# Performance work log

Measured on AMD Instinct MI355X. Metric: run time of the kernel, lower is better.

## Reference

```python
import jax, jax.numpy as jnp
import numpy as np

H = 64  # rnn_hidden_size


def _rnn_seq(x, W_ih, W_hh, b_ih, b_hh):
    """One tanh RNN layer over [B,T,D] -> full output sequence [B,T,H]."""
    pre = jnp.einsum('btd,hd->bth', x, W_ih) + b_ih  # input projection hoisted out of the scan
    h0 = jnp.zeros((x.shape[0], W_hh.shape[0]), x.dtype)
    def step(h, p_t):
        h = jnp.tanh(p_t + h @ W_hh.T + b_hh)
        return h, h
    _, ys = jax.lax.scan(step, h0, jnp.swapaxes(pre, 0, 1))  # scan over time
    return jnp.swapaxes(ys, 0, 1)


def _rnn_last(x, W_ih, W_hh, b_ih, b_hh):
    """One tanh RNN layer, returning only the last hidden state [B,H]."""
    pre = jnp.einsum('btd,hd->bth', x, W_ih) + b_ih
    h0 = jnp.zeros((x.shape[0], W_hh.shape[0]), x.dtype)
    def step(h, p_t):
        return jnp.tanh(p_t + h @ W_hh.T + b_hh), None
    h, _ = jax.lax.scan(step, h0, jnp.swapaxes(pre, 0, 1))
    return h


def setup_inputs() -> dict:
    key = jax.random.key(0)
    ks = jax.random.split(key, 32)
    B, T, D = 128, 4096, 3
    kr = 1.0 / np.sqrt(H)          # PyTorch RNN init bound
    u = lambda kk, shape, b: jax.random.uniform(kk, shape, jnp.float32, -b, b)
    inp = {
        'x': jax.random.normal(ks[0], (B, T, D), jnp.float32),
        'y': jax.random.normal(ks[1], (B, T, D), jnp.float32),
        'z': jax.random.normal(ks[2], (5,), jnp.float32),
        # rnn_empty, layer 0 (in=3) and layer 1 (in=64)
        'e_Wih0': u(ks[3], (H, D), kr), 'e_Whh0': u(ks[4], (H, H), kr),
        'e_bih0': u(ks[5], (H,), kr),  'e_bhh0': u(ks[6], (H,), kr),
        'e_Wih1': u(ks[7], (H, H), kr), 'e_Whh1': u(ks[8], (H, H), kr),
        'e_bih1': u(ks[9], (H,), kr),  'e_bhh1': u(ks[10], (H,), kr),
        # rnn_occupied
        'o_Wih0': u(ks[11], (H, D), kr), 'o_Whh0': u(ks[12], (H, H), kr),
        'o_bih0': u(ks[13], (H,), kr),  'o_bhh0': u(ks[14], (H,), kr),
        'o_Wih1': u(ks[15], (H, H), kr), 'o_Whh1': u(ks[16], (H, H), kr),
        'o_bih1': u(ks[17], (H,), kr),  'o_bhh1': u(ks[18], (H,), kr),
        # heads: fce/fco (64->2), fc1 (9->64), fc2 (64->5)
        'fce_w': u(ks[19], (2, H), kr), 'fce_b': u(ks[20], (2,), kr),
        'fco_w': u(ks[21], (2, H), kr), 'fco_b': u(ks[22], (2,), kr),
        'fc1_w': u(ks[23], (64, 9), 1.0 / np.sqrt(9)), 'fc1_b': u(ks[24], (64,), 1.0 / np.sqrt(9)),
        'fc2_w': u(ks[25], (5, 64), kr), 'fc2_b': u(ks[26], (5,), kr),
    }
    return inp


def reference(x, y, z,
              e_Wih0, e_Whh0, e_bih0, e_bhh0, e_Wih1, e_Whh1, e_bih1, e_bhh1,
              o_Wih0, o_Whh0, o_bih0, o_bhh0, o_Wih1, o_Whh1, o_bih1, o_bhh1,
              fce_w, fce_b, fco_w, fco_b, fc1_w, fc1_b, fc2_w, fc2_b):
    # two 2-layer tanh RNNs; last-timestep output of layer 2 == final hidden of layer 2
    hx = _rnn_last(_rnn_seq(x, e_Wih0, e_Whh0, e_bih0, e_bhh0),
                   e_Wih1, e_Whh1, e_bih1, e_bhh1)            # [B,H]
    hy = _rnn_last(_rnn_seq(y, o_Wih0, o_Whh0, o_bih0, o_bhh0),
                   o_Wih1, o_Whh1, o_bih1, o_bhh1)            # [B,H]
    e = hx @ fce_w.T + fce_b                                  # [B,2]
    o = hy @ fco_w.T + fco_b                                  # [B,2]
    zz = jnp.concatenate([e[0], o[0], z])                     # [9]
    h = jax.nn.relu(zz @ fc1_w.T + fc1_b)                     # [64]
    return h @ fc2_w.T + fc2_b                                # [5]
```

## Files before the change

kernel.cpp:

```cpp
#include <hip/hip_runtime.h>

#define T 4096
#define EP 8
#define RING 32
#define NEP (T / EP + 2)

__device__ __forceinline__ float fast_tanh(float x) {
    float e = __expf(2.0f * x);
    float r = __builtin_amdgcn_rcpf(e + 1.0f);
    return fmaf(-2.0f, r, 1.0f);
}

__device__ __forceinline__ float lane_bcast(float v, int j) {
    return __uint_as_float(__builtin_amdgcn_readlane(__float_as_uint(v), j));
}

#define ANCHOR16(a, b) asm volatile("" : \
    "+v"((a)[(b)+0]),  "+v"((a)[(b)+1]),  "+v"((a)[(b)+2]),  "+v"((a)[(b)+3]),  \
    "+v"((a)[(b)+4]),  "+v"((a)[(b)+5]),  "+v"((a)[(b)+6]),  "+v"((a)[(b)+7]),  \
    "+v"((a)[(b)+8]),  "+v"((a)[(b)+9]),  "+v"((a)[(b)+10]), "+v"((a)[(b)+11]), \
    "+v"((a)[(b)+12]), "+v"((a)[(b)+13]), "+v"((a)[(b)+14]), "+v"((a)[(b)+15]))
#define ANCHOR64(a) do { ANCHOR16(a, 0); ANCHOR16(a, 16); \
                         ANCHOR16(a, 32); ANCHOR16(a, 48); } while (0)

__global__ void prep_kernel(const float* __restrict__ x, const float* __restrict__ y,
                            const float* __restrict__ eW, const float* __restrict__ ebi,
                            const float* __restrict__ ebh,
                            const float* __restrict__ oW, const float* __restrict__ obi,
                            const float* __restrict__ obh,
                            float* __restrict__ pre)
{
    int idx = blockIdx.x * blockDim.x + threadIdx.x;
    int i = idx & 63;
    int t = (idx >> 6) & (T - 1);
    int s = idx >> 18;
    const float* in = s ? y : x;
    const float* W  = s ? oW : eW;
    const float* bi = s ? obi : ebi;
    const float* bh = s ? obh : ebh;
    float v = bi[i] + bh[i]
            + W[i*3+0]*in[t*3+0] + W[i*3+1]*in[t*3+1] + W[i*3+2]*in[t*3+2];
    pre[idx] = v;
}

__global__ __launch_bounds__(256, 1) void seq_kernel(
    const float* __restrict__ pre,
    const float* __restrict__ eWhh0, const float* __restrict__ eWih1,
    const float* __restrict__ eWhh1, const float* __restrict__ ebih1,
    const float* __restrict__ ebhh1,
    const float* __restrict__ oWhh0, const float* __restrict__ oWih1,
    const float* __restrict__ oWhh1, const float* __restrict__ obih1,
    const float* __restrict__ obhh1,
    float* __restrict__ hlast)
{
    const int s    = blockIdx.x;
    const int wv   = threadIdx.x >> 6;
    const int lane = threadIdx.x & 63;

    __shared__ __align__(16) float h0ring[RING][64];
    __shared__ __align__(16) float qring[RING][64];

    const float* p = pre + s * T * 64;

    if (wv == 0) {
        const float* Whh0 = s ? oWhh0 : eWhh0;
        float w0[64];
#pragma unroll
        for (int j = 0; j < 64; ++j) w0[j] = Whh0[lane * 64 + j];

        float hp = 0.f;
        float pc[EP], pn[EP];
#pragma unroll
        for (int i = 0; i < EP; ++i) pc[i] = p[i * 64 + lane];

        for (int k = 0; k < NEP; ++k) {
            ANCHOR64(w0);
            const int base = k * EP;
#pragma unroll
            for (int i = 0; i < EP; ++i) {
                int t = base + EP + i;
                pn[i] = (t < T) ? p[t * 64 + lane] : 0.f;
            }
            if (base < T) {
#pragma unroll
                for (int i = 0; i < EP; ++i) {
                    float aa[4] = { pc[i], 0.f, 0.f, 0.f };
#pragma unroll
                    for (int jb = 0; jb < 64; jb += 8) {
                        float hj[8];
#pragma unroll
                        for (int u = 0; u < 8; ++u) hj[u] = lane_bcast(hp, jb + u);
#pragma unroll
                        for (int u = 0; u < 8; ++u)
                            aa[u & 3] = fmaf(w0[jb + u], hj[u], aa[u & 3]);
                    }
                    hp = fast_tanh((aa[0] + aa[1]) + (aa[2] + aa[3]));
                    h0ring[(base + i) & (RING - 1)][lane] = hp;
                }
            }
#pragma unroll
            for (int i = 0; i < EP; ++i) pc[i] = pn[i];
            __syncthreads();
        }
    } else if (wv <= 2) {
        const float* Wih1 = s ? oWih1 : eWih1;
        const float  b1   = s ? (obih1[lane] + obhh1[lane])
                              : (ebih1[lane] + ebhh1[lane]);
        float wi[64];
#pragma unroll
        for (int j = 0; j < 64; ++j) wi[j] = Wih1[lane * 64 + j];

        const int i0 = (wv - 1) * (EP / 2);

        for (int k = 0; k < NEP; ++k) {
            ANCHOR64(wi);
            const int base = k * EP - EP;
            if (base >= 0 && base < T) {
#pragma unroll
                for (int i = 0; i < EP / 2; ++i) {
                    const int t = base + i0 + i;
                    const float4* hv = (const float4*)h0ring[t & (RING - 1)];
                    float q[4] = { b1, 0.f, 0.f, 0.f };
#pragma unroll
                    for (int j4 = 0; j4 < 16; ++j4) {
                        float4 u = hv[j4];
                        q[0] = fmaf(wi[4*j4+0], u.x, q[0]);
                        q[1] = fmaf(wi[4*j4+1], u.y, q[1]);
                        q[2] = fmaf(wi[4*j4+2], u.z, q[2]);
                        q[3] = fmaf(wi[4*j4+3], u.w, q[3]);
                    }
                    qring[t & (RING - 1)][lane] = (q[0] + q[1]) + (q[2] + q[3]);
                }
            }
            __syncthreads();
        }
    } else {
        const float* Whh1 = s ? oWhh1 : eWhh1;
        float w1[64];
#pragma unroll
        for (int j = 0; j < 64; ++j) w1[j] = Whh1[lane * 64 + j];

        float hp = 0.f;
        for (int k = 0; k < NEP; ++k) {
            ANCHOR64(w1);
            const int base = k * EP - 2 * EP;
            if (base >= 0) {
                float qb[EP];
#pragma unroll
                for (int i = 0; i < EP; ++i)
                    qb[i] = qring[(base + i) & (RING - 1)][lane];
#pragma unroll
                for (int i = 0; i < EP; ++i) {
                    float cc[4] = { qb[i], 0.f, 0.f, 0.f };
#pragma unroll
                    for (int jb = 0; jb < 64; jb += 8) {
                        float hj[8];
#pragma unroll
                        for (int u = 0; u < 8; ++u) hj[u] = lane_bcast(hp, jb + u);
#pragma unroll
                        for (int u = 0; u < 8; ++u)
                            cc[u & 3] = fmaf(w1[jb + u], hj[u], cc[u & 3]);
                    }
                    hp = fast_tanh((cc[0] + cc[1]) + (cc[2] + cc[3]));
                }
            }
            __syncthreads();
        }
        hlast[s * 64 + lane] = hp;
    }
}

__global__ void head_kernel(const float* __restrict__ hlast,
                            const float* __restrict__ z,
                            const float* __restrict__ fce_w, const float* __restrict__ fce_b,
                            const float* __restrict__ fco_w, const float* __restrict__ fco_b,
                            const float* __restrict__ fc1_w, const float* __restrict__ fc1_b,
                            const float* __restrict__ fc2_w, const float* __restrict__ fc2_b,
                            float* __restrict__ out)
{
    const int lane = threadIdx.x;
    __shared__ float zz[9];
    __shared__ float hh[64];

    if (lane < 2) {
        float sacc = fce_b[lane];
        for (int j = 0; j < 64; ++j) sacc += fce_w[lane * 64 + j] * hlast[j];
        zz[lane] = sacc;
    } else if (lane < 4) {
        int r = lane - 2;
        float sacc = fco_b[r];
        for (int j = 0; j < 64; ++j) sacc += fco_w[r * 64 + j] * hlast[64 + j];
        zz[lane] = sacc;
    } else if (lane < 9) {
        zz[lane] = z[lane - 4];
    }
    __syncthreads();

    float sacc = fc1_b[lane];
#pragma unroll
    for (int j = 0; j < 9; ++j) sacc += fc1_w[lane * 9 + j] * zz[j];
    hh[lane] = fmaxf(sacc, 0.f);
    __syncthreads();

    if (lane < 5) {
        float o = fc2_b[lane];
        for (int i = 0; i < 64; ++i) o += fc2_w[lane * 64 + i] * hh[i];
        out[lane] = o;
    }
}

extern "C" void kernel_launch(void* const* d_in, const int* in_sizes, int n_in,
                              void* d_out, int out_size, void* d_ws, size_t ws_size,
                              hipStream_t stream)
{
    const float* x      = (const float*)d_in[0];
    const float* y      = (const float*)d_in[1];
    const float* z      = (const float*)d_in[2];
    const float* e_Wih0 = (const float*)d_in[3];
    const float* e_Whh0 = (const float*)d_in[4];
    const float* e_bih0 = (const float*)d_in[5];
    const float* e_bhh0 = (const float*)d_in[6];
    const float* e_Wih1 = (const float*)d_in[7];
    const float* e_Whh1 = (const float*)d_in[8];
    const float* e_bih1 = (const float*)d_in[9];
    const float* e_bhh1 = (const float*)d_in[10];
    const float* o_Wih0 = (const float*)d_in[11];
    const float* o_Whh0 = (const float*)d_in[12];
    const float* o_bih0 = (const float*)d_in[13];
    const float* o_bhh0 = (const float*)d_in[14];
    const float* o_Wih1 = (const float*)d_in[15];
    const float* o_Whh1 = (const float*)d_in[16];
    const float* o_bih1 = (const float*)d_in[17];
    const float* o_bhh1 = (const float*)d_in[18];
    const float* fce_w  = (const float*)d_in[19];
    const float* fce_b  = (const float*)d_in[20];
    const float* fco_w  = (const float*)d_in[21];
    const float* fco_b  = (const float*)d_in[22];
    const float* fc1_w  = (const float*)d_in[23];
    const float* fc1_b  = (const float*)d_in[24];
    const float* fc2_w  = (const float*)d_in[25];
    const float* fc2_b  = (const float*)d_in[26];

    float* pre   = (float*)d_ws;
    float* hlast = pre + 2 * T * 64;
    float* out   = (float*)d_out;

    prep_kernel<<<(2 * T * 64) / 256, 256, 0, stream>>>(
        x, y, e_Wih0, e_bih0, e_bhh0, o_Wih0, o_bih0, o_bhh0, pre);

    seq_kernel<<<2, 256, 0, stream>>>(
        pre,
        e_Whh0, e_Wih1, e_Whh1, e_bih1, e_bhh1,
        o_Whh0, o_Wih1, o_Whh1, o_bih1, o_bhh1,
        hlast);

    head_kernel<<<1, 64, 0, stream>>>(
        hlast, z, fce_w, fce_b, fco_w, fco_b, fc1_w, fc1_b, fc2_w, fc2_b, out);
}
```

Measured before the change: 1.104 ms.

## Replace readlane broadcasts with DPP row-rotate and bpermute in recurrent matvec

The per-step recurrent matvec previously broadcast each of the 64 hidden values with v_readlane into scalar registers, which serializes through SGPRs. It now rotates the hidden vector within 16-lane rows using DPP row_ror fused into the FMAs, and fetches the other three 16-lane quarters with ds_bpermute. The weights are pre-permuted per lane so each rotation matches the right column. The direction of the DPP rotation is detected at runtime to pick the permutation. This adds LDS-crossbar latency from the bpermutes on the serial critical path, plus the risk that the rotation semantics are wrong.

```diff
diff --git a/kernel.cpp b/kernel.cpp
--- a/kernel.cpp
+++ b/kernel.cpp
@@ -9,10 +9,6 @@
     float e = __expf(2.0f * x);
     float r = __builtin_amdgcn_rcpf(e + 1.0f);
     return fmaf(-2.0f, r, 1.0f);
-}
-
-__device__ __forceinline__ float lane_bcast(float v, int j) {
-    return __uint_as_float(__builtin_amdgcn_readlane(__float_as_uint(v), j));
 }
 
 #define ANCHOR16(a, b) asm volatile("" : \
@@ -22,6 +18,47 @@
     "+v"((a)[(b)+12]), "+v"((a)[(b)+13]), "+v"((a)[(b)+14]), "+v"((a)[(b)+15]))
 #define ANCHOR64(a) do { ANCHOR16(a, 0); ANCHOR16(a, 16); \
                          ANCHOR16(a, 32); ANCHOR16(a, 48); } while (0)
+
+#define ROTF(acc, v, w, R) \
+    (acc) = fmaf(__int_as_float(__builtin_amdgcn_update_dpp( \
+        0, __float_as_int(v), 0x120 + (R), 0xF, 0xF, false)), (w), (acc))
+
+#define KBLOCK(v, wd, B) do { \
+    a0 = fmaf((v), (wd)[(B) + 0], a0); \
+    ROTF(a1, (v), (wd)[(B) + 1],  1);  ROTF(a2, (v), (wd)[(B) + 2],  2); \
+    ROTF(a3, (v), (wd)[(B) + 3],  3);  ROTF(a0, (v), (wd)[(B) + 4],  4); \
+    ROTF(a1, (v), (wd)[(B) + 5],  5);  ROTF(a2, (v), (wd)[(B) + 6],  6); \
+    ROTF(a3, (v), (wd)[(B) + 7],  7);  ROTF(a0, (v), (wd)[(B) + 8],  8); \
+    ROTF(a1, (v), (wd)[(B) + 9],  9);  ROTF(a2, (v), (wd)[(B) +10], 10); \
+    ROTF(a3, (v), (wd)[(B) +11], 11);  ROTF(a0, (v), (wd)[(B) +12], 12); \
+    ROTF(a1, (v), (wd)[(B) +13], 13);  ROTF(a2, (v), (wd)[(B) +14], 14); \
+    ROTF(a3, (v), (wd)[(B) +15], 15); \
+} while (0)
+
+__device__ __forceinline__ float rnn_step_dpp(const float (&wd)[64], float init, float hp,
+                                              int a16, int a32, int a48) {
+    const int hb = __float_as_int(hp);
+    const int b1i = __builtin_amdgcn_ds_bpermute(a16, hb);
+    const int b2i = __builtin_amdgcn_ds_bpermute(a32, hb);
+    const int b3i = __builtin_amdgcn_ds_bpermute(a48, hb);
+    float a0 = init, a1 = 0.f, a2 = 0.f, a3 = 0.f;
+    KBLOCK(hp, wd, 0);
+    const float v1 = __int_as_float(b1i); KBLOCK(v1, wd, 16);
+    const float v2 = __int_as_float(b2i); KBLOCK(v2, wd, 32);
+    const float v3 = __int_as_float(b3i); KBLOCK(v3, wd, 48);
+    return fast_tanh((a0 + a1) + (a2 + a3));
+}
+
+__device__ __forceinline__ void load_wdpp(const float* __restrict__ W, int lane,
+                                          bool dirplus, float (&wd)[64]) {
+#pragma unroll
+    for (int m = 0; m < 64; ++m) {
+        const int k = m >> 4, r = m & 15;
+        const int lowoff = dirplus ? r : ((16 - r) & 15);
+        const int j = ((lane & 48) | ((lane + lowoff) & 15)) ^ (k << 4);
+        wd[m] = W[lane * 64 + j];
+    }
+}
 
 __global__ void prep_kernel(const float* __restrict__ x, const float* __restrict__ y,
                             const float* __restrict__ eW, const float* __restrict__ ebi,
@@ -62,11 +99,16 @@
 
     const float* p = pre + s * T * 64;
 
+    const int got = __builtin_amdgcn_update_dpp(0, lane, 0x121, 0xF, 0xF, false);
+    const bool dirplus = ((got & 15) == ((lane + 1) & 15));
+    const int a16 = (lane ^ 16) << 2;
+    const int a32 = (lane ^ 32) << 2;
+    const int a48 = (lane ^ 48) << 2;
+
     if (wv == 0) {
         const float* Whh0 = s ? oWhh0 : eWhh0;
-        float w0[64];
-#pragma unroll
-        for (int j = 0; j < 64; ++j) w0[j] = Whh0[lane * 64 + j];
+        float wd[64];
+        load_wdpp(Whh0, lane, dirplus, wd);
 
         float hp = 0.f;
         float pc[EP], pn[EP];
@@ -74,7 +116,7 @@
         for (int i = 0; i < EP; ++i) pc[i] = p[i * 64 + lane];
 
         for (int k = 0; k < NEP; ++k) {
-            ANCHOR64(w0);
+            ANCHOR64(wd);
             const int base = k * EP;
 #pragma unroll
             for (int i = 0; i < EP; ++i) {
@@ -84,17 +126,7 @@
             if (base < T) {
 #pragma unroll
                 for (int i = 0; i < EP; ++i) {
-                    float aa[4] = { pc[i], 0.f, 0.f, 0.f };
-#pragma unroll
-                    for (int jb = 0; jb < 64; jb += 8) {
-                        float hj[8];
-#pragma unroll
-                        for (int u = 0; u < 8; ++u) hj[u] = lane_bcast(hp, jb + u);
-#pragma unroll
-                        for (int u = 0; u < 8; ++u)
-                            aa[u & 3] = fmaf(w0[jb + u], hj[u], aa[u & 3]);
-                    }
-                    hp = fast_tanh((aa[0] + aa[1]) + (aa[2] + aa[3]));
+                    hp = rnn_step_dpp(wd, pc[i], hp, a16, a32, a48);
                     h0ring[(base + i) & (RING - 1)][lane] = hp;
                 }
             }
@@ -136,13 +168,12 @@
         }
     } else {
         const float* Whh1 = s ? oWhh1 : eWhh1;
-        float w1[64];
-#pragma unroll
-        for (int j = 0; j < 64; ++j) w1[j] = Whh1[lane * 64 + j];
+        float wd[64];
+        load_wdpp(Whh1, lane, dirplus, wd);
 
         float hp = 0.f;
         for (int k = 0; k < NEP; ++k) {
-            ANCHOR64(w1);
+            ANCHOR64(wd);
             const int base = k * EP - 2 * EP;
             if (base >= 0) {
                 float qb[EP];
@@ -150,19 +181,8 @@
                 for (int i = 0; i < EP; ++i)
                     qb[i] = qring[(base + i) & (RING - 1)][lane];
 #pragma unroll
-                for (int i = 0; i < EP; ++i) {
-                    float cc[4] = { qb[i], 0.f, 0.f, 0.f };
-#pragma unroll
-                    for (int jb = 0; jb < 64; jb += 8) {
-                        float hj[8];
-#pragma unroll
-                        for (int u = 0; u < 8; ++u) hj[u] = lane_bcast(hp, jb + u);
-#pragma unroll
-                        for (int u = 0; u < 8; ++u)
-                            cc[u & 3] = fmaf(w1[jb + u], hj[u], cc[u & 3]);
-                    }
-                    hp = fast_tanh((cc[0] + cc[1]) + (cc[2] + cc[3]));
-                }
+                for (int i = 0; i < EP; ++i)
+                    hp = rnn_step_dpp(wd, qb[i], hp, a16, a32, a48);
             }
             __syncthreads();
         }
```

Measured after the change: 1.513 ms. 1.37x slower.
